# Optimization experiments

Measured on AMD Instinct MI355X. Metric: run time of the kernel, lower is better.

The kernel has to match this reference:

```python
import jax, jax.numpy as jnp
import numpy as np

S, B, HQ, HKV, D = 2048, 2, 32, 8, 128
SCALE = 1.0 / np.sqrt(D).astype(np.float32)  # scale_factor = 1/sqrt(head_dim)


def setup_inputs() -> dict:
    key = jax.random.key(0)
    kq, kk, kv = jax.random.split(key, 3)
    return {
        "query": jax.random.normal(kq, (S, B, HQ, D), dtype=jnp.float32),
        "key": jax.random.normal(kk, (S, B, HKV, D), dtype=jnp.float32),
        "value": jax.random.normal(kv, (S, B, HKV, D), dtype=jnp.float32),
    }


def reference(query, key, value):
    # GQA: reshape query into [S, B, h_kv, group, D]
    group = HQ // HKV
    gq = query.reshape(S, B, HKV, group, D)
    # logits: [B, h_kv, group, Sq, Sk]
    logits = jnp.einsum("qbhgd,kbhd->bhgqk", gq, key) * jnp.float32(SCALE)
    # scaled upper-triangular (causal) masked softmax
    causal = jnp.tril(jnp.ones((S, S), dtype=bool))  # allow k <= q
    logits = jnp.where(causal[None, None, None], logits, jnp.finfo(jnp.float32).min)
    attn = jax.nn.softmax(logits, axis=-1)
    out = jnp.einsum("bhgqk,kbhd->qbhgd", attn, value)
    return out.reshape(S, B, HQ, D)
```

## Files before the change

kernel.cpp:

```cpp
#include <hip/hip_runtime.h>

#define SEQ    2048
#define BATCH  2
#define NHQ    32
#define NHKV   8
#define DHEAD  128
#define QSCALE 0.08838834764831845f

typedef __fp16 f16;
typedef f16 f16x2 __attribute__((ext_vector_type(2)));
typedef f16 f16x4 __attribute__((ext_vector_type(4)));
typedef f16 f16x8 __attribute__((ext_vector_type(8)));
typedef float f32x4 __attribute__((ext_vector_type(4)));

#define KSTRIDE 136
#define VSTRIDE 40
#define KBUF    (32 * KSTRIDE)
#define VBUF    (128 * VSTRIDE)

__global__ __launch_bounds__(512, 4) void attn_fwd(const float* __restrict__ Q,
                                                   const float* __restrict__ K,
                                                   const float* __restrict__ V,
                                                   float* __restrict__ O) {
  const int bh  = blockIdx.y;
  const int b   = bh >> 5;
  const int hq  = bh & 31;
  const int hkv = hq >> 2;
  const int t    = threadIdx.x;
  const int wave = t >> 6;
  const int lane = t & 63;
  const int col  = lane & 15;
  const int quad = lane >> 4;

  const int qrs = BATCH * NHQ * DHEAD;
  const int krs = BATCH * NHKV * DHEAD;

  const float* Qp = Q + ((size_t)b * NHQ  + hq ) * DHEAD;
  const float* Kp = K + ((size_t)b * NHKV + hkv) * DHEAD;
  const float* Vp = V + ((size_t)b * NHKV + hkv) * DHEAD;
  float*       Op = O + ((size_t)b * NHQ  + hq ) * DHEAD;

  __shared__ __align__(16) f16 smem[2 * KBUF + 2 * VBUF];

  const int ktk = t >> 5;
  const int ktd = (t & 31) * 4;
  const int vd  = t & 127;
  const int vh  = t >> 7;

  #pragma unroll 1
  for (int pass = 0; pass < 2; ++pass) {
    const int qt     = pass ? (int)blockIdx.x : 15 - (int)blockIdx.x;
    const int q_base = qt * 128 + wave * 16;

    f16x8 qf[4];
    {
      const float* qsrc = Qp + (size_t)(q_base + col) * qrs + quad * 8;
      #pragma unroll
      for (int c = 0; c < 4; ++c) {
        float4 a = *(const float4*)(qsrc + c * 32);
        float4 e = *(const float4*)(qsrc + c * 32 + 4);
        f16x2 p0 = __builtin_amdgcn_cvt_pkrtz(a.x * QSCALE, a.y * QSCALE);
        f16x2 p1 = __builtin_amdgcn_cvt_pkrtz(a.z * QSCALE, a.w * QSCALE);
        f16x2 p2 = __builtin_amdgcn_cvt_pkrtz(e.x * QSCALE, e.y * QSCALE);
        f16x2 p3 = __builtin_amdgcn_cvt_pkrtz(e.z * QSCALE, e.w * QSCALE);
        qf[c][0] = p0[0]; qf[c][1] = p0[1]; qf[c][2] = p1[0]; qf[c][3] = p1[1];
        qf[c][4] = p2[0]; qf[c][5] = p2[1]; qf[c][6] = p3[0]; qf[c][7] = p3[1];
      }
    }

    f32x4 oacc[8];
    #pragma unroll
    for (int h = 0; h < 8; ++h) oacc[h] = (f32x4){0.f, 0.f, 0.f, 0.f};
    float m_i = -__builtin_inff();
    float l_i = 0.f;

    const int nt_blk = 4 * qt + 4;
    const int nt_w   = 4 * qt + (wave >> 1) + 1;

    float4 kr[2];
    float  vf[8];

    #pragma unroll
    for (int ro = 0; ro < 2; ++ro)
      kr[ro] = *(const float4*)(Kp + (size_t)(ktk + ro * 16) * krs + ktd);
    #pragma unroll
    for (int i = 0; i < 8; ++i)
      vf[i] = Vp[(size_t)(vh * 8 + i) * krs + vd];

    for (int kt = 0; kt < nt_blk; ++kt) {
      const int bf = kt & 1;
      f16* kb = smem + bf * KBUF;
      f16* vb = smem + 2 * KBUF + bf * VBUF;

      #pragma unroll
      for (int ro = 0; ro < 2; ++ro) {
        f16x2 lo = __builtin_amdgcn_cvt_pkrtz(kr[ro].x, kr[ro].y);
        f16x2 hi = __builtin_amdgcn_cvt_pkrtz(kr[ro].z, kr[ro].w);
        f16x4 v4; v4[0] = lo[0]; v4[1] = lo[1]; v4[2] = hi[0]; v4[3] = hi[1];
        *(f16x4*)(kb + (ktk + ro * 16) * KSTRIDE + ktd) = v4;
      }
      {
        f16x2 p0 = __builtin_amdgcn_cvt_pkrtz(vf[0], vf[1]);
        f16x2 p1 = __builtin_amdgcn_cvt_pkrtz(vf[2], vf[3]);
        f16x2 p2 = __builtin_amdgcn_cvt_pkrtz(vf[4], vf[5]);
        f16x2 p3 = __builtin_amdgcn_cvt_pkrtz(vf[6], vf[7]);
        f16x8 v8;
        v8[0] = p0[0]; v8[1] = p0[1]; v8[2] = p1[0]; v8[3] = p1[1];
        v8[4] = p2[0]; v8[5] = p2[1]; v8[6] = p3[0]; v8[7] = p3[1];
        *(f16x8*)(vb + vd * VSTRIDE + vh * 8) = v8;
      }

      if (kt + 1 < nt_blk) {
        const int k0n = (kt + 1) * 32;
        #pragma unroll
        for (int ro = 0; ro < 2; ++ro)
          kr[ro] = *(const float4*)(Kp + (size_t)(k0n + ktk + ro * 16) * krs + ktd);
        #pragma unroll
        for (int i = 0; i < 8; ++i)
          vf[i] = Vp[(size_t)(k0n + vh * 8 + i) * krs + vd];
      }

      __syncthreads();

      if (kt < nt_w) {
        const int k0 = kt * 32;

        f32x4 s0 = {0.f, 0.f, 0.f, 0.f}, s1 = {0.f, 0.f, 0.f, 0.f};
        #pragma unroll
        for (int c = 0; c < 4; ++c) {
          f16x8 ka = *(const f16x8*)(kb + col * KSTRIDE + quad * 8 + c * 32);
          s0 = __builtin_amdgcn_mfma_f32_16x16x32_f16(ka, qf[c], s0, 0, 0, 0);
        }
        #pragma unroll
        for (int c = 0; c < 4; ++c) {
          f16x8 ka = *(const f16x8*)(kb + (16 + col) * KSTRIDE + quad * 8 + c * 32);
          s1 = __builtin_amdgcn_mfma_f32_16x16x32_f16(ka, qf[c], s1, 0, 0, 0);
        }

        const int qrow = q_base + col;
        if (k0 + 31 > q_base) {
          #pragma unroll
          for (int r = 0; r < 4; ++r) {
            if (k0 + quad * 4 + r      > qrow) s0[r] = -__builtin_inff();
            if (k0 + 16 + quad * 4 + r > qrow) s1[r] = -__builtin_inff();
          }
        }

        float mx = fmaxf(fmaxf(fmaxf(s0[0], s0[1]), fmaxf(s0[2], s0[3])),
                         fmaxf(fmaxf(s1[0], s1[1]), fmaxf(s1[2], s1[3])));
        mx = fmaxf(mx, __shfl_xor(mx, 16, 64));
        mx = fmaxf(mx, __shfl_xor(mx, 32, 64));

        if (!__all(mx - m_i <= 8.0f)) {
          const float mnew  = fmaxf(m_i, mx);
          const float alpha = __expf(m_i - mnew);
          m_i = mnew;
          l_i *= alpha;
          #pragma unroll
          for (int h = 0; h < 8; ++h) {
            oacc[h][0] *= alpha; oacc[h][1] *= alpha;
            oacc[h][2] *= alpha; oacc[h][3] *= alpha;
          }
        }

        float e0[4], e1[4], rs = 0.f;
        #pragma unroll
        for (int r = 0; r < 4; ++r) {
          e0[r] = __expf(s0[r] - m_i);
          e1[r] = __expf(s1[r] - m_i);
          rs += e0[r] + e1[r];
        }
        rs += __shfl_xor(rs, 16, 64);
        rs += __shfl_xor(rs, 32, 64);
        l_i += rs;

        f16x2 a01 = __builtin_amdgcn_cvt_pkrtz(e0[0], e0[1]);
        f16x2 a23 = __builtin_amdgcn_cvt_pkrtz(e0[2], e0[3]);
        f16x2 b01 = __builtin_amdgcn_cvt_pkrtz(e1[0], e1[1]);
        f16x2 b23 = __builtin_amdgcn_cvt_pkrtz(e1[2], e1[3]);
        f16x4 pb0; pb0[0] = a01[0]; pb0[1] = a01[1]; pb0[2] = a23[0]; pb0[3] = a23[1];
        f16x4 pb1; pb1[0] = b01[0]; pb1[1] = b01[1]; pb1[2] = b23[0]; pb1[3] = b23[1];

        #pragma unroll
        for (int h = 0; h < 8; ++h) {
          const f16* vr = vb + (h * 16 + col) * VSTRIDE + quad * 4;
          f16x4 va0 = *(const f16x4*)(vr);
          f16x4 va1 = *(const f16x4*)(vr + 16);
          oacc[h] = __builtin_amdgcn_mfma_f32_16x16x16f16(va0, pb0, oacc[h], 0, 0, 0);
          oacc[h] = __builtin_amdgcn_mfma_f32_16x16x16f16(va1, pb1, oacc[h], 0, 0, 0);
        }
      }
    }

    {
      const float invl = 1.0f / l_i;
      #pragma unroll
      for (int h = 0; h < 8; ++h) {
        float4 o;
        o.x = oacc[h][0] * invl; o.y = oacc[h][1] * invl;
        o.z = oacc[h][2] * invl; o.w = oacc[h][3] * invl;
        *(float4*)(Op + (size_t)(q_base + col) * qrs + h * 16 + quad * 4) = o;
      }
    }
  }
}

extern "C" void kernel_launch(void* const* d_in, const int* in_sizes, int n_in,
                              void* d_out, int out_size, void* d_ws, size_t ws_size,
                              hipStream_t stream) {
  const float* Q = (const float*)d_in[0];
  const float* K = (const float*)d_in[1];
  const float* V = (const float*)d_in[2];
  float* O = (float*)d_out;
  (void)in_sizes; (void)n_in; (void)out_size; (void)d_ws; (void)ws_size;
  dim3 grid(SEQ / 256, BATCH * NHQ);
  attn_fwd<<<grid, dim3(512), 0, stream>>>(Q, K, V, O);
}
```

Baseline: 258.7 us.

## Use 16x16x32 MFMA for PV via permuted K rows and exp2 softmax

Permutes the K tile's row order in shared memory so each lane's score elements line up with a contiguous 8-key slice. This lets the PV product use one 16x16x32 f16 MFMA per head chunk instead of two 16x16x16 MFMAs, with a single 8-wide LDS read of V. The causal mask indices are remapped to match. The log2(e) factor is also folded into the Q scale so the softmax can use native exp2 instead of __expf, removing a multiply per exponent.

```diff
diff --git a/kernel.cpp b/kernel.cpp
--- a/kernel.cpp
+++ b/kernel.cpp
@@ -5,7 +5,7 @@
 #define NHQ    32
 #define NHKV   8
 #define DHEAD  128
-#define QSCALE 0.08838834764831845f
+#define QSCALE2 0.12751743f
 
 typedef __fp16 f16;
 typedef f16 f16x2 __attribute__((ext_vector_type(2)));
@@ -17,6 +17,14 @@
 #define VSTRIDE 40
 #define KBUF    (32 * KSTRIDE)
 #define VBUF    (128 * VSTRIDE)
+
+static __device__ __forceinline__ float fast_exp2(float x) {
+#if __has_builtin(__builtin_amdgcn_exp2f)
+  return __builtin_amdgcn_exp2f(x);
+#else
+  return __builtin_exp2f(x);
+#endif
+}
 
 __global__ __launch_bounds__(512, 4) void attn_fwd(const float* __restrict__ Q,
                                                    const float* __restrict__ K,
@@ -46,6 +54,7 @@
   const int ktd = (t & 31) * 4;
   const int vd  = t & 127;
   const int vh  = t >> 7;
+  const int klr = ((ktk >> 2) & 1) * 16 + (ktk >> 3) * 4 + (ktk & 3);
 
   #pragma unroll 1
   for (int pass = 0; pass < 2; ++pass) {
@@ -59,10 +68,10 @@
       for (int c = 0; c < 4; ++c) {
         float4 a = *(const float4*)(qsrc + c * 32);
         float4 e = *(const float4*)(qsrc + c * 32 + 4);
-        f16x2 p0 = __builtin_amdgcn_cvt_pkrtz(a.x * QSCALE, a.y * QSCALE);
-        f16x2 p1 = __builtin_amdgcn_cvt_pkrtz(a.z * QSCALE, a.w * QSCALE);
-        f16x2 p2 = __builtin_amdgcn_cvt_pkrtz(e.x * QSCALE, e.y * QSCALE);
-        f16x2 p3 = __builtin_amdgcn_cvt_pkrtz(e.z * QSCALE, e.w * QSCALE);
+        f16x2 p0 = __builtin_amdgcn_cvt_pkrtz(a.x * QSCALE2, a.y * QSCALE2);
+        f16x2 p1 = __builtin_amdgcn_cvt_pkrtz(a.z * QSCALE2, a.w * QSCALE2);
+        f16x2 p2 = __builtin_amdgcn_cvt_pkrtz(e.x * QSCALE2, e.y * QSCALE2);
+        f16x2 p3 = __builtin_amdgcn_cvt_pkrtz(e.z * QSCALE2, e.w * QSCALE2);
         qf[c][0] = p0[0]; qf[c][1] = p0[1]; qf[c][2] = p1[0]; qf[c][3] = p1[1];
         qf[c][4] = p2[0]; qf[c][5] = p2[1]; qf[c][6] = p3[0]; qf[c][7] = p3[1];
       }
@@ -97,7 +106,7 @@
         f16x2 lo = __builtin_amdgcn_cvt_pkrtz(kr[ro].x, kr[ro].y);
         f16x2 hi = __builtin_amdgcn_cvt_pkrtz(kr[ro].z, kr[ro].w);
         f16x4 v4; v4[0] = lo[0]; v4[1] = lo[1]; v4[2] = hi[0]; v4[3] = hi[1];
-        *(f16x4*)(kb + (ktk + ro * 16) * KSTRIDE + ktd) = v4;
+        *(f16x4*)(kb + (klr + ro * 8) * KSTRIDE + ktd) = v4;
       }
       {
         f16x2 p0 = __builtin_amdgcn_cvt_pkrtz(vf[0], vf[1]);
@@ -141,8 +150,8 @@
         if (k0 + 31 > q_base) {
           #pragma unroll
           for (int r = 0; r < 4; ++r) {
-            if (k0 + quad * 4 + r      > qrow) s0[r] = -__builtin_inff();
-            if (k0 + 16 + quad * 4 + r > qrow) s1[r] = -__builtin_inff();
+            if (k0 + quad * 8 + r     > qrow) s0[r] = -__builtin_inff();
+            if (k0 + quad * 8 + 4 + r > qrow) s1[r] = -__builtin_inff();
           }
         }
 
@@ -153,7 +162,7 @@
 
         if (!__all(mx - m_i <= 8.0f)) {
           const float mnew  = fmaxf(m_i, mx);
-          const float alpha = __expf(m_i - mnew);
+          const float alpha = fast_exp2(m_i - mnew);
           m_i = mnew;
           l_i *= alpha;
           #pragma unroll
@@ -166,8 +175,8 @@
         float e0[4], e1[4], rs = 0.f;
         #pragma unroll
         for (int r = 0; r < 4; ++r) {
-          e0[r] = __expf(s0[r] - m_i);
-          e1[r] = __expf(s1[r] - m_i);
+          e0[r] = fast_exp2(s0[r] - m_i);
+          e1[r] = fast_exp2(s1[r] - m_i);
           rs += e0[r] + e1[r];
         }
         rs += __shfl_xor(rs, 16, 64);
@@ -178,16 +187,14 @@
         f16x2 a23 = __builtin_amdgcn_cvt_pkrtz(e0[2], e0[3]);
         f16x2 b01 = __builtin_amdgcn_cvt_pkrtz(e1[0], e1[1]);
         f16x2 b23 = __builtin_amdgcn_cvt_pkrtz(e1[2], e1[3]);
-        f16x4 pb0; pb0[0] = a01[0]; pb0[1] = a01[1]; pb0[2] = a23[0]; pb0[3] = a23[1];
-        f16x4 pb1; pb1[0] = b01[0]; pb1[1] = b01[1]; pb1[2] = b23[0]; pb1[3] = b23[1];
+        f16x8 pb;
+        pb[0] = a01[0]; pb[1] = a01[1]; pb[2] = a23[0]; pb[3] = a23[1];
+        pb[4] = b01[0]; pb[5] = b01[1]; pb[6] = b23[0]; pb[7] = b23[1];
 
         #pragma unroll
         for (int h = 0; h < 8; ++h) {
-          const f16* vr = vb + (h * 16 + col) * VSTRIDE + quad * 4;
-          f16x4 va0 = *(const f16x4*)(vr);
-          f16x4 va1 = *(const f16x4*)(vr + 16);
-          oacc[h] = __builtin_amdgcn_mfma_f32_16x16x16f16(va0, pb0, oacc[h], 0, 0, 0);
-          oacc[h] = __builtin_amdgcn_mfma_f32_16x16x16f16(va1, pb1, oacc[h], 0, 0, 0);
+          f16x8 va = *(const f16x8*)(vb + (h * 16 + col) * VSTRIDE + quad * 8);
+          oacc[h] = __builtin_amdgcn_mfma_f32_16x16x32_f16(va, pb, oacc[h], 0, 0, 0);
         }
       }
     }
```

After: 245.2 us. 5.2% less time.
